# Optimization experiments

Hardware: AMD Instinct MI355X
Metric: run time of the kernel (lower is better)

Reference implementation:

```python
import jax, jax.numpy as jnp
import numpy as np

N = 100_000      # nodes
E = 1_600_000    # edges
F_IN = 64        # num_features
H = 64           # hidden_dim
G = 128          # graphs in batch
BN_EPS = 1e-5


def _gcn_conv(x, W, b, row, col, ew, n_nodes):
    """PyG GCNConv with edge weights, self-loops, symmetric normalization."""
    # add self loops (weight 1.0)
    loops = jnp.arange(n_nodes, dtype=row.dtype)
    r = jnp.concatenate([row, loops])
    c = jnp.concatenate([col, loops])
    w = jnp.concatenate([ew, jnp.ones((n_nodes,), ew.dtype)])
    # deg over destination (col), as in PyG gcn_norm
    deg = jax.ops.segment_sum(w, c, num_segments=n_nodes)
    dinv = jnp.where(deg > 0, jax.lax.rsqrt(deg), 0.0)
    norm = dinv[r] * w * dinv[c]          # [E+N]
    h = x @ W                             # [N, H] small GEMM
    msg = h[r] * norm[:, None]            # gather + scale, [E+N, H]
    out = jax.ops.segment_sum(msg, c, num_segments=n_nodes)  # scatter-add
    return out + b


def _bn_eval(x, gamma, beta, mean, var):
    return (x - mean) * jax.lax.rsqrt(var + BN_EPS) * gamma + beta


def setup_inputs() -> dict:
    key = jax.random.key(0)
    ks = jax.random.split(key, 10)
    x = jax.random.normal(ks[0], (N, F_IN), jnp.float32)
    edge_index = jax.random.randint(ks[1], (2, E), 0, N, dtype=jnp.int32)
    edge_weight = jax.random.uniform(ks[2], (E,), jnp.float32)
    batch = jnp.sort(jax.random.randint(ks[3], (N,), 0, G, dtype=jnp.int32))

    def lin(k, i, o):
        return jax.random.normal(k, (i, o), jnp.float32) / np.float32(np.sqrt(i))

    d = {
        "x": x, "edge_index": edge_index, "edge_weight": edge_weight, "batch": batch,
        "W1": lin(ks[4], F_IN, H), "b1": jnp.zeros((H,), jnp.float32),
        "W2": lin(ks[5], H, H),    "b2": jnp.zeros((H,), jnp.float32),
        "W3": lin(ks[6], H, H),    "b3": jnp.zeros((H,), jnp.float32),
        "Wfc": lin(ks[7], H, 1),   "bfc": jnp.zeros((1,), jnp.float32),
    }
    for i in (1, 2, 3):
        d[f"g{i}"] = jnp.ones((H,), jnp.float32)   # BN gamma
        d[f"be{i}"] = jnp.zeros((H,), jnp.float32)  # BN beta
        d[f"m{i}"] = jnp.zeros((H,), jnp.float32)   # BN running mean
        d[f"v{i}"] = jnp.ones((H,), jnp.float32)    # BN running var
    return d


def reference(x, edge_index, edge_weight, batch,
              W1, b1, W2, b2, W3, b3, Wfc, bfc,
              g1, be1, m1, v1, g2, be2, m2, v2, g3, be3, m3, v3):
    row, col = edge_index[0], edge_index[1]
    h = _gcn_conv(x, W1, b1, row, col, edge_weight, N)
    h = _bn_eval(jax.nn.relu(h), g1, be1, m1, v1)
    h = _gcn_conv(h, W2, b2, row, col, edge_weight, N)
    h = _bn_eval(jax.nn.relu(h), g2, be2, m2, v2)
    h = _gcn_conv(h, W3, b3, row, col, edge_weight, N)
    h = _bn_eval(h, g3, be3, m3, v3)               # note: no ReLU before bn3
    pooled = jax.ops.segment_sum(h, batch, num_segments=G)  # global_add_pool
    pooled = jax.nn.relu(pooled)                   # dropout is identity in eval
    return (pooled @ Wfc + bfc).reshape(-1)        # [G]
```

## Files before the change

### kernel.cpp

```cpp
#include <hip/hip_runtime.h>
#include <hip/hip_fp16.h>

#define BN_EPS 1e-5f
#define EPB 4096
#define PADCAP 4608
#define FP8_SCALE 16.0f
#define FP8_INV (1.0f / 16.0f)
#define W15_INV (1.0f / 32768.0f)
#define NPOOL 8

typedef __attribute__((ext_vector_type(2))) float vfloat2;
typedef __attribute__((ext_vector_type(8))) short short8;
typedef __attribute__((ext_vector_type(4))) float f32x4;

__device__ __forceinline__ float fatomic_add(float* p, float v) {
    return unsafeAtomicAdd(p, v);
}

__device__ __forceinline__ unsigned short f2bf(float f) {
    unsigned int u = __float_as_uint(f);
    return (unsigned short)((u + 0x7FFFu + ((u >> 16) & 1u)) >> 16);
}

__device__ __forceinline__ int xcd_swz(int bid, int nwg) {
    int xcd = bid & 7, k = bid >> 3;
    int q = nwg >> 3, r = nwg & 7;
    return (xcd < r ? xcd * (q + 1) : r * (q + 1) + (xcd - r) * q) + k;
}

__global__ __launch_bounds__(256) void k_wt(const float* __restrict__ W1,
                                            const float* __restrict__ W2,
                                            const float* __restrict__ W3,
                                            short* __restrict__ WT) {
    int tid = threadIdx.x;
    const float* Wm[3] = {W1, W2, W3};
#pragma unroll
    for (int m = 0; m < 3; ++m) {
        const float* W = Wm[m];
        short* o = WT + m * 4096;
        for (int i = tid; i < 4096; i += 256)
            o[i] = (short)f2bf(W[(i & 63) * 64 + (i >> 6)]);
    }
}

__global__ __launch_bounds__(256) void k_binscatter(const int* __restrict__ rowi,
                                                    const int* __restrict__ coli,
                                                    const float* __restrict__ ew,
                                                    unsigned int* __restrict__ binCursor,
                                                    int2* __restrict__ staged,
                                                    float* __restrict__ pooled8,
                                                    int E, int NB, int PZ) {
    __shared__ unsigned int h[512];
    __shared__ unsigned int bb[512];
    int tid = threadIdx.x;
    if (blockIdx.x == 0)
        for (int i = tid; i < PZ; i += 256) pooled8[i] = 0.f;
    for (int i = tid; i < 512; i += 256) h[i] = 0;
    __syncthreads();
    int base = blockIdx.x * EPB;
    int lim = min(EPB, E - base);
    unsigned short rank[16];
    int nj = (lim - tid + 255) / 256;
    for (int j = 0; j < nj; ++j) {
        int e = base + tid + j * 256;
        rank[j] = (unsigned short)atomicAdd(&h[(unsigned)coli[e] >> 8], 1u);
    }
    __syncthreads();
    for (int b = tid; b < NB; b += 256)
        bb[b] = h[b] ? atomicAdd(&binCursor[b], h[b]) : 0u;
    __syncthreads();
    for (int j = 0; j < nj; ++j) {
        int e = base + tid + j * 256;
        unsigned int c = (unsigned)coli[e];
        unsigned int b = c >> 8;
        int2 rec;
        rec.x = rowi[e] | (int)((c & 255u) << 24);
        rec.y = (int)min((unsigned int)(ew[e] * 32768.f + 0.5f), 32767u);
        staged[(size_t)b * PADCAP + bb[b] + rank[j]] = rec;
    }
}

__global__ __launch_bounds__(256) void k_binfinal(const int2* __restrict__ staged,
                                                  const unsigned int* __restrict__ binCursor,
                                                  unsigned int* __restrict__ csr,
                                                  int2* __restrict__ se,
                                                  float* __restrict__ dinv,
                                                  int N) {
    __shared__ int2 recs[PADCAP];
    __shared__ unsigned int cnt[256];
    __shared__ unsigned int deg[256];
    __shared__ int sc[256];
    __shared__ unsigned int cur[256];
    int tid = threadIdx.x;
    int b = blockIdx.x;
    int s0 = b * PADCAP;
    int n = (int)binCursor[b];
    cnt[tid] = 0;
    deg[tid] = 0;
    __syncthreads();
    for (int i = tid; i < n; i += 256) {
        int2 rec = staged[s0 + i];
        recs[i] = rec;
        unsigned int cl = (unsigned)rec.x >> 24;
        atomicAdd(&cnt[cl], 1u);
        atomicAdd(&deg[cl], (unsigned int)rec.y);
    }
    __syncthreads();
    int v = (int)cnt[tid];
    sc[tid] = v;
    __syncthreads();
    for (int off = 1; off < 256; off <<= 1) {
        int add = (tid >= off) ? sc[tid - off] : 0;
        __syncthreads();
        sc[tid] += add;
        __syncthreads();
    }
    int lpre = sc[tid] - v;
    cur[tid] = (unsigned int)lpre;
    int c = b * 256 + tid;
    if (c < N) {
        se[c] = make_int2(s0 + lpre, s0 + lpre + v);
        dinv[c] = rsqrtf(1.0f + (float)deg[tid] * W15_INV);
    }
    __syncthreads();
    for (int i = tid; i < n; i += 256) {
        int2 rec = recs[i];
        unsigned int cl = (unsigned)rec.x >> 24;
        unsigned int p = atomicAdd(&cur[cl], 1u);
        csr[s0 + p] = ((unsigned int)rec.y << 17) | ((unsigned)rec.x & 0x1FFFFu);
    }
}

__global__ __launch_bounds__(256) void k_gemm(const float* __restrict__ x,
                                              const short* __restrict__ WTg,
                                              const float* __restrict__ dinv,
                                              int* __restrict__ th4, int n) {
    __shared__ short Wt[64][72];
    __shared__ short xs[16][72];
    __shared__ float outs[16][68];
    int tid = threadIdx.x;
    {
        const int* WTi = (const int*)WTg;
        for (int i = tid; i < 2048; i += 256)
            *(int*)&Wt[i >> 5][(i & 31) * 2] = WTi[i];
    }
    int row0 = blockIdx.x * 16;
    int nrows = min(16, n - row0);
    {
        int r = tid >> 4, c4 = (tid & 15) * 4;
        float4 v = make_float4(0.f, 0.f, 0.f, 0.f);
        if (r < nrows)
            v = ((const float4*)(x + (size_t)(row0 + r) * 64))[tid & 15];
        xs[r][c4 + 0] = (short)f2bf(v.x);
        xs[r][c4 + 1] = (short)f2bf(v.y);
        xs[r][c4 + 2] = (short)f2bf(v.z);
        xs[r][c4 + 3] = (short)f2bf(v.w);
    }
    __syncthreads();
    int wv = tid >> 6, lane = tid & 63;
    int mn = lane & 15, kg = (lane >> 4) * 8;
    f32x4 acc = {0.f, 0.f, 0.f, 0.f};
    short8 a0 = *(const short8*)&xs[mn][kg];
    short8 a1 = *(const short8*)&xs[mn][kg + 32];
    short8 b0 = *(const short8*)&Wt[wv * 16 + mn][kg];
    short8 b1 = *(const short8*)&Wt[wv * 16 + mn][kg + 32];
    acc = __builtin_amdgcn_mfma_f32_16x16x32_bf16(a0, b0, acc, 0, 0, 0);
    acc = __builtin_amdgcn_mfma_f32_16x16x32_bf16(a1, b1, acc, 0, 0, 0);
#pragma unroll
    for (int r = 0; r < 4; ++r)
        outs[(lane >> 4) * 4 + r][wv * 16 + mn] = acc[r];
    __syncthreads();
    int rl = tid >> 4, fq = tid & 15;
    if (rl < nrows) {
        float d = dinv[row0 + rl] * FP8_SCALE;
        float4 o = *(const float4*)&outs[rl][fq * 4];
        int p = __builtin_amdgcn_cvt_pk_fp8_f32(o.x * d, o.y * d, 0, false);
        p = __builtin_amdgcn_cvt_pk_fp8_f32(o.z * d, o.w * d, p, true);
        th4[(row0 + rl) * 16 + fq] = p;
    }
}

__global__ __launch_bounds__(256) void k_fusedgg(const unsigned int* __restrict__ csr,
                                                 const int2* __restrict__ se,
                                                 const int* __restrict__ th4_in,
                                                 const float* __restrict__ dinv,
                                                 const float* __restrict__ bias,
                                                 const float* __restrict__ gam,
                                                 const float* __restrict__ bet,
                                                 const float* __restrict__ mu,
                                                 const float* __restrict__ var,
                                                 const short* __restrict__ WTg,
                                                 int* __restrict__ th4_out, int n) {
    __shared__ short Wt[64][72];
    __shared__ short xs[16][72];
    __shared__ float outs[16][68];
    int tid = threadIdx.x;
    {
        const int* WTi = (const int*)WTg;
        for (int i = tid; i < 2048; i += 256)
            *(int*)&Wt[i >> 5][(i & 31) * 2] = WTi[i];
    }
    int nb = xcd_swz(blockIdx.x, gridDim.x);
    int w = tid >> 6;
    int lane = tid & 63;
    int q = lane >> 4;
    int l = lane & 15;
    int node = nb * 16 + w * 4 + q;
    bool valid = node < n;
    float4 b4 = ((const float4*)bias)[l];
    float4 m4 = ((const float4*)mu)[l];
    float4 v4 = ((const float4*)var)[l];
    float4 G4 = ((const float4*)gam)[l];
    float4 B4 = ((const float4*)bet)[l];
    float4 scf, shf;
    scf.x = rsqrtf(v4.x + BN_EPS) * G4.x;  shf.x = B4.x - m4.x * scf.x;
    scf.y = rsqrtf(v4.y + BN_EPS) * G4.y;  shf.y = B4.y - m4.y * scf.y;
    scf.z = rsqrtf(v4.z + BN_EPS) * G4.z;  shf.z = B4.z - m4.z * scf.z;
    scf.w = rsqrtf(v4.w + BN_EPS) * G4.w;  shf.w = B4.w - m4.w * scf.w;

    float4 av[4];
    av[0] = make_float4(0.f, 0.f, 0.f, 0.f);
    av[1] = av[0]; av[2] = av[0]; av[3] = av[0];
    float4 sf = av[0];
    int e = 0, eend = 0;
    float dv = 0.f;
    if (valid) {
        int2 ext = se[node];
        e = ext.x; eend = ext.y;
        dv = dinv[node];
        int sv = th4_in[node * 16 + l];
        vfloat2 lo = __builtin_amdgcn_cvt_pk_f32_fp8(sv, false);
        vfloat2 hi = __builtin_amdgcn_cvt_pk_f32_fp8(sv, true);
        sf = make_float4(lo.x, lo.y, hi.x, hi.y);
    }
    while (__any(e < eend)) {
        if (e < eend) {
            unsigned int cc[8];
            int rr[8];
#pragma unroll
            for (int j = 0; j < 8; ++j)
                cc[j] = __builtin_nontemporal_load(&csr[e + j]);
#pragma unroll
            for (int j = 0; j < 8; ++j)
                rr[j] = th4_in[(int)((cc[j] & 0x1FFFFu) << 4) + l];
#pragma unroll
            for (int j = 0; j < 8; ++j) {
                float wj = (e + j < eend) ? (float)(cc[j] >> 17) : 0.f;
                vfloat2 lo = __builtin_amdgcn_cvt_pk_f32_fp8(rr[j], false);
                vfloat2 hi = __builtin_amdgcn_cvt_pk_f32_fp8(rr[j], true);
                av[j & 3].x = fmaf(wj, lo.x, av[j & 3].x);
                av[j & 3].y = fmaf(wj, lo.y, av[j & 3].y);
                av[j & 3].z = fmaf(wj, hi.x, av[j & 3].z);
                av[j & 3].w = fmaf(wj, hi.y, av[j & 3].w);
            }
        }
        e += 8;
    }
    float4 res = make_float4(0.f, 0.f, 0.f, 0.f);
    if (valid) {
        float4 acc;
        acc.x = ((av[0].x + av[1].x) + (av[2].x + av[3].x)) * W15_INV + sf.x;
        acc.y = ((av[0].y + av[1].y) + (av[2].y + av[3].y)) * W15_INV + sf.y;
        acc.z = ((av[0].z + av[1].z) + (av[2].z + av[3].z)) * W15_INV + sf.z;
        acc.w = ((av[0].w + av[1].w) + (av[2].w + av[3].w)) * W15_INV + sf.w;
        float d = dv * FP8_INV;
        float r0 = fmaxf(d * acc.x + b4.x, 0.f);
        float r1 = fmaxf(d * acc.y + b4.y, 0.f);
        float r2 = fmaxf(d * acc.z + b4.z, 0.f);
        float r3 = fmaxf(d * acc.w + b4.w, 0.f);
        res.x = r0 * scf.x + shf.x;
        res.y = r1 * scf.y + shf.y;
        res.z = r2 * scf.z + shf.z;
        res.w = r3 * scf.w + shf.w;
    }
    {
        int nl = w * 4 + q;
        union { unsigned short s[4]; int2 i2; } u;
        u.s[0] = f2bf(res.x); u.s[1] = f2bf(res.y);
        u.s[2] = f2bf(res.z); u.s[3] = f2bf(res.w);
        *(int2*)&xs[nl][4 * l] = u.i2;
    }
    __syncthreads();
    int mn = lane & 15, kg = (lane >> 4) * 8;
    f32x4 acc = {0.f, 0.f, 0.f, 0.f};
    short8 a0 = *(const short8*)&xs[mn][kg];
    short8 a1 = *(const short8*)&xs[mn][kg + 32];
    short8 b0 = *(const short8*)&Wt[w * 16 + mn][kg];
    short8 b1 = *(const short8*)&Wt[w * 16 + mn][kg + 32];
    acc = __builtin_amdgcn_mfma_f32_16x16x32_bf16(a0, b0, acc, 0, 0, 0);
    acc = __builtin_amdgcn_mfma_f32_16x16x32_bf16(a1, b1, acc, 0, 0, 0);
#pragma unroll
    for (int r = 0; r < 4; ++r)
        outs[(lane >> 4) * 4 + r][w * 16 + mn] = acc[r];
    __syncthreads();
    int rl = tid >> 4, fq = tid & 15;
    int row = nb * 16 + rl;
    if (row < n) {
        float d = dinv[row] * FP8_SCALE;
        float4 o = *(const float4*)&outs[rl][fq * 4];
        int p = __builtin_amdgcn_cvt_pk_fp8_f32(o.x * d, o.y * d, 0, false);
        p = __builtin_amdgcn_cvt_pk_fp8_f32(o.z * d, o.w * d, p, true);
        th4_out[row * 16 + fq] = p;
    }
}

__global__ __launch_bounds__(256) void k_gather(const unsigned int* __restrict__ csr,
                                                const int2* __restrict__ se,
                                                const int* __restrict__ th4,
                                                const float* __restrict__ dinv,
                                                const float* __restrict__ bias,
                                                const float* __restrict__ gam,
                                                const float* __restrict__ bet,
                                                const float* __restrict__ mu,
                                                const float* __restrict__ var,
                                                const int* __restrict__ batch,
                                                float* __restrict__ pooled8,
                                                int n, int G64) {
    __shared__ float vals[4][64];
    __shared__ int wbid[4];
    int nb = xcd_swz(blockIdx.x, gridDim.x);
    int w = threadIdx.x >> 6;
    int lane = threadIdx.x & 63;
    int q = lane >> 4;
    int l = lane & 15;
    int node = nb * 16 + w * 4 + q;
    bool valid = node < n;
    float* myPool = pooled8 + (size_t)(blockIdx.x & (NPOOL - 1)) * G64;
    float4 b4 = ((const float4*)bias)[l];
    float4 m4 = ((const float4*)mu)[l];
    float4 v4 = ((const float4*)var)[l];
    float4 G4 = ((const float4*)gam)[l];
    float4 B4 = ((const float4*)bet)[l];
    float4 scf, shf;
    scf.x = rsqrtf(v4.x + BN_EPS) * G4.x;  shf.x = B4.x - m4.x * scf.x;
    scf.y = rsqrtf(v4.y + BN_EPS) * G4.y;  shf.y = B4.y - m4.y * scf.y;
    scf.z = rsqrtf(v4.z + BN_EPS) * G4.z;  shf.z = B4.z - m4.z * scf.z;
    scf.w = rsqrtf(v4.w + BN_EPS) * G4.w;  shf.w = B4.w - m4.w * scf.w;

    float4 av[4];
    av[0] = make_float4(0.f, 0.f, 0.f, 0.f);
    av[1] = av[0]; av[2] = av[0]; av[3] = av[0];
    float4 sf = av[0];
    int e = 0, eend = 0;
    float dv = 0.f;
    if (valid) {
        int2 ext = se[node];
        e = ext.x; eend = ext.y;
        dv = dinv[node];
        int sv = th4[node * 16 + l];
        vfloat2 lo = __builtin_amdgcn_cvt_pk_f32_fp8(sv, false);
        vfloat2 hi = __builtin_amdgcn_cvt_pk_f32_fp8(sv, true);
        sf = make_float4(lo.x, lo.y, hi.x, hi.y);
    }
    while (__any(e < eend)) {
        if (e < eend) {
            unsigned int cc[8];
            int rr[8];
#pragma unroll
            for (int j = 0; j < 8; ++j)
                cc[j] = __builtin_nontemporal_load(&csr[e + j]);
#pragma unroll
            for (int j = 0; j < 8; ++j)
                rr[j] = th4[(int)((cc[j] & 0x1FFFFu) << 4) + l];
#pragma unroll
            for (int j = 0; j < 8; ++j) {
                float wj = (e + j < eend) ? (float)(cc[j] >> 17) : 0.f;
                vfloat2 lo = __builtin_amdgcn_cvt_pk_f32_fp8(rr[j], false);
                vfloat2 hi = __builtin_amdgcn_cvt_pk_f32_fp8(rr[j], true);
                av[j & 3].x = fmaf(wj, lo.x, av[j & 3].x);
                av[j & 3].y = fmaf(wj, lo.y, av[j & 3].y);
                av[j & 3].z = fmaf(wj, hi.x, av[j & 3].z);
                av[j & 3].w = fmaf(wj, hi.y, av[j & 3].w);
            }
        }
        e += 8;
    }
    float4 res = make_float4(0.f, 0.f, 0.f, 0.f);
    if (valid) {
        float4 acc;
        acc.x = ((av[0].x + av[1].x) + (av[2].x + av[3].x)) * W15_INV + sf.x;
        acc.y = ((av[0].y + av[1].y) + (av[2].y + av[3].y)) * W15_INV + sf.y;
        acc.z = ((av[0].z + av[1].z) + (av[2].z + av[3].z)) * W15_INV + sf.z;
        acc.w = ((av[0].w + av[1].w) + (av[2].w + av[3].w)) * W15_INV + sf.w;
        float d = dv * FP8_INV;
        float r0 = d * acc.x + b4.x;
        float r1 = d * acc.y + b4.y;
        float r2 = d * acc.z + b4.z;
        float r3 = d * acc.w + b4.w;
        res.x = r0 * scf.x + shf.x;
        res.y = r1 * scf.y + shf.y;
        res.z = r2 * scf.z + shf.z;
        res.w = r3 * scf.w + shf.w;
    }
    int bid = valid ? batch[node] : -1;
    int bid0 = __shfl(bid, 0);
    bool same = __all(bid == bid0);
    if (same) {
        res.x += __shfl_xor(res.x, 16);
        res.y += __shfl_xor(res.y, 16);
        res.z += __shfl_xor(res.z, 16);
        res.w += __shfl_xor(res.w, 16);
        res.x += __shfl_xor(res.x, 32);
        res.y += __shfl_xor(res.y, 32);
        res.z += __shfl_xor(res.z, 32);
        res.w += __shfl_xor(res.w, 32);
        if (q == 0) ((float4*)&vals[w][0])[l] = res;
        if (lane == 0) wbid[w] = bid0;
    } else {
        if (valid) {
            float* pp = myPool + bid * 64 + 4 * l;
            fatomic_add(pp + 0, res.x);
            fatomic_add(pp + 1, res.y);
            fatomic_add(pp + 2, res.z);
            fatomic_add(pp + 3, res.w);
        }
        if (lane == 0) wbid[w] = -1;
    }
    __syncthreads();
    if (w == 0) {
        int f = threadIdx.x;
        float s2 = 0.f;
        int cur = -1;
#pragma unroll
        for (int i = 0; i < 4; ++i) {
            int bi = wbid[i];
            if (bi < 0) continue;
            if (bi == cur) {
                s2 += vals[i][f];
            } else {
                if (cur >= 0) fatomic_add(&myPool[cur * 64 + f], s2);
                cur = bi;
                s2 = vals[i][f];
            }
        }
        if (cur >= 0) fatomic_add(&myPool[cur * 64 + f], s2);
    }
}

__global__ __launch_bounds__(64) void k_fc(const float* __restrict__ pooled8,
                                           const float* __restrict__ Wfc,
                                           const float* __restrict__ bfc,
                                           float* __restrict__ out, int G) {
    int g = blockIdx.x;
    int f = threadIdx.x;
    int G64 = G * 64;
    float p = 0.f;
#pragma unroll
    for (int c = 0; c < NPOOL; ++c) p += pooled8[c * G64 + g * 64 + f];
    float s = fmaxf(p, 0.f) * Wfc[f];
#pragma unroll
    for (int off = 1; off < 64; off <<= 1) s += __shfl_xor(s, off);
    if (f == 0) out[g] = s + bfc[0];
}

extern "C" void kernel_launch(void* const* d_in, const int* in_sizes, int n_in,
                              void* d_out, int out_size, void* d_ws, size_t ws_size,
                              hipStream_t stream) {
    const float* x    = (const float*)d_in[0];
    const int*   eidx = (const int*)d_in[1];
    const float* ew   = (const float*)d_in[2];
    const int*   batch= (const int*)d_in[3];
    const float* W1 = (const float*)d_in[4];
    const float* b1 = (const float*)d_in[5];
    const float* W2 = (const float*)d_in[6];
    const float* b2 = (const float*)d_in[7];
    const float* W3 = (const float*)d_in[8];
    const float* b3 = (const float*)d_in[9];
    const float* Wfc = (const float*)d_in[10];
    const float* bfc = (const float*)d_in[11];
    const float* g1 = (const float*)d_in[12];
    const float* be1 = (const float*)d_in[13];
    const float* m1 = (const float*)d_in[14];
    const float* v1 = (const float*)d_in[15];
    const float* g2 = (const float*)d_in[16];
    const float* be2 = (const float*)d_in[17];
    const float* m2 = (const float*)d_in[18];
    const float* v2 = (const float*)d_in[19];
    const float* g3 = (const float*)d_in[20];
    const float* be3 = (const float*)d_in[21];
    const float* m3 = (const float*)d_in[22];
    const float* v3 = (const float*)d_in[23];

    const int N = in_sizes[0] / 64;
    const int E = in_sizes[1] / 2;
    const int G = out_size;
    const int* rowi = eidx;
    const int* coli = eidx + E;
    const int NB = (N + 255) >> 8;

    char* ws = (char*)d_ws;
    size_t off = 0;
    auto alloc = [&](size_t bytes) {
        char* p = ws + off;
        off += (bytes + 255) & ~(size_t)255;
        return p;
    };
    unsigned int* binCursor = (unsigned int*)alloc(512 * 4);
    float* dinv   = (float*)alloc((size_t)N * 4);
    int2*  se     = (int2*) alloc((size_t)N * 8);
    unsigned int* csr = (unsigned int*)alloc((size_t)NB * PADCAP * 4 + 256);
    int*   th4a   = (int*)  alloc((size_t)N * 64);
    int*   th4b   = (int*)  alloc((size_t)N * 64);
    float* pooled8 = (float*)alloc((size_t)NPOOL * G * 64 * 4);
    short* wtg    = (short*)alloc(3 * 4096 * 2);
    int2*  staged = (int2*)alloc((size_t)NB * PADCAP * 8);

    const int bblk = (E + EPB - 1) / EPB;
    const int gblk = (N + 15) / 16;
    const int mblk = (N + 15) / 16;

    k_wt<<<1, 256, 0, stream>>>(W1, W2, W3, wtg);
    hipMemsetAsync(binCursor, 0, 512 * 4, stream);
    k_binscatter<<<bblk, 256, 0, stream>>>(rowi, coli, ew, binCursor, staged,
                                           pooled8, E, NB, NPOOL * G * 64);
    k_binfinal<<<NB, 256, 0, stream>>>(staged, binCursor, csr, se, dinv, N);

    k_gemm<<<mblk, 256, 0, stream>>>(x, wtg, dinv, th4a, N);
    k_fusedgg<<<gblk, 256, 0, stream>>>(csr, se, th4a, dinv, b1, g1, be1, m1, v1,
                                        wtg + 4096, th4b, N);
    k_fusedgg<<<gblk, 256, 0, stream>>>(csr, se, th4b, dinv, b2, g2, be2, m2, v2,
                                        wtg + 8192, th4a, N);
    k_gather<<<gblk, 256, 0, stream>>>(csr, se, th4a, dinv, b3, g3, be3, m3, v3,
                                       batch, pooled8, N, G * 64);
    k_fc<<<G, 64, 0, stream>>>(pooled8, Wfc, bfc, (float*)d_out, G);
}
```

Measured before the change: 310.4 us.

## Locally sort edges by bin in LDS before coalesced staged writes; fuse weight transpose

In the bin-scatter kernel, each block now runs a prefix scan over its per-bin counts and places its edges into a shared-memory buffer sorted by bin. It then writes them to the staged array in contiguous runs, replacing scattered 8-byte global stores with mostly coalesced ones. The bin id is packed into the weight field so the copy-out loop can find each record's destination, and the consumer masks those bits off. The separate weight-transpose kernel launch is folded into block 1 of this kernel, at the cost of extra LDS (about 32KB), which may lower occupancy.

```diff
diff --git a/kernel.cpp b/kernel.cpp
--- a/kernel.cpp
+++ b/kernel.cpp
@@ -28,33 +28,35 @@
     return (xcd < r ? xcd * (q + 1) : r * (q + 1) + (xcd - r) * q) + k;
 }
 
-__global__ __launch_bounds__(256) void k_wt(const float* __restrict__ W1,
-                                            const float* __restrict__ W2,
-                                            const float* __restrict__ W3,
-                                            short* __restrict__ WT) {
-    int tid = threadIdx.x;
-    const float* Wm[3] = {W1, W2, W3};
-#pragma unroll
-    for (int m = 0; m < 3; ++m) {
-        const float* W = Wm[m];
-        short* o = WT + m * 4096;
-        for (int i = tid; i < 4096; i += 256)
-            o[i] = (short)f2bf(W[(i & 63) * 64 + (i >> 6)]);
-    }
-}
-
 __global__ __launch_bounds__(256) void k_binscatter(const int* __restrict__ rowi,
                                                     const int* __restrict__ coli,
                                                     const float* __restrict__ ew,
                                                     unsigned int* __restrict__ binCursor,
                                                     int2* __restrict__ staged,
                                                     float* __restrict__ pooled8,
+                                                    const float* __restrict__ W1,
+                                                    const float* __restrict__ W2,
+                                                    const float* __restrict__ W3,
+                                                    short* __restrict__ WT,
                                                     int E, int NB, int PZ) {
     __shared__ unsigned int h[512];
-    __shared__ unsigned int bb[512];
+    __shared__ unsigned int lo[512];
+    __shared__ unsigned int dd[512];
+    __shared__ unsigned int ps[256];
+    __shared__ int2 lsorted[EPB];
     int tid = threadIdx.x;
-    if (blockIdx.x == 0)
+    if (blockIdx.x == 0) {
         for (int i = tid; i < PZ; i += 256) pooled8[i] = 0.f;
+    } else if (blockIdx.x == 1) {
+        const float* Wm[3] = {W1, W2, W3};
+#pragma unroll
+        for (int m = 0; m < 3; ++m) {
+            const float* W = Wm[m];
+            short* o = WT + m * 4096;
+            for (int i = tid; i < 4096; i += 256)
+                o[i] = (short)f2bf(W[(i & 63) * 64 + (i >> 6)]);
+        }
+    }
     for (int i = tid; i < 512; i += 256) h[i] = 0;
     __syncthreads();
     int base = blockIdx.x * EPB;
@@ -66,8 +68,23 @@
         rank[j] = (unsigned short)atomicAdd(&h[(unsigned)coli[e] >> 8], 1u);
     }
     __syncthreads();
-    for (int b = tid; b < NB; b += 256)
-        bb[b] = h[b] ? atomicAdd(&binCursor[b], h[b]) : 0u;
+    unsigned int a0 = h[2 * tid], a1 = h[2 * tid + 1];
+    ps[tid] = a0 + a1;
+    __syncthreads();
+    for (int off = 1; off < 256; off <<= 1) {
+        unsigned int add = (tid >= off) ? ps[tid - off] : 0u;
+        __syncthreads();
+        ps[tid] += add;
+        __syncthreads();
+    }
+    unsigned int excl = ps[tid] - (a0 + a1);
+    lo[2 * tid] = excl;
+    lo[2 * tid + 1] = excl + a0;
+    __syncthreads();
+    for (int b = tid; b < NB; b += 256) {
+        unsigned int bbv = h[b] ? atomicAdd(&binCursor[b], h[b]) : 0u;
+        dd[b] = (unsigned int)(b * PADCAP) + bbv - lo[b];
+    }
     __syncthreads();
     for (int j = 0; j < nj; ++j) {
         int e = base + tid + j * 256;
@@ -75,8 +92,15 @@
         unsigned int b = c >> 8;
         int2 rec;
         rec.x = rowi[e] | (int)((c & 255u) << 24);
-        rec.y = (int)min((unsigned int)(ew[e] * 32768.f + 0.5f), 32767u);
-        staged[(size_t)b * PADCAP + bb[b] + rank[j]] = rec;
+        unsigned int w15 = min((unsigned int)(ew[e] * 32768.f + 0.5f), 32767u);
+        rec.y = (int)(w15 | (b << 15));
+        lsorted[lo[b] + rank[j]] = rec;
+    }
+    __syncthreads();
+    for (int i = tid; i < lim; i += 256) {
+        int2 rec = lsorted[i];
+        unsigned int b = ((unsigned)rec.y >> 15) & 0x1FFu;
+        staged[dd[b] + i] = rec;
     }
 }
 
@@ -103,7 +127,7 @@
         recs[i] = rec;
         unsigned int cl = (unsigned)rec.x >> 24;
         atomicAdd(&cnt[cl], 1u);
-        atomicAdd(&deg[cl], (unsigned int)rec.y);
+        atomicAdd(&deg[cl], (unsigned int)rec.y & 0x7FFFu);
     }
     __syncthreads();
     int v = (int)cnt[tid];
@@ -127,7 +151,8 @@
         int2 rec = recs[i];
         unsigned int cl = (unsigned)rec.x >> 24;
         unsigned int p = atomicAdd(&cur[cl], 1u);
-        csr[s0 + p] = ((unsigned int)rec.y << 17) | ((unsigned)rec.x & 0x1FFFFu);
+        csr[s0 + p] = (((unsigned int)rec.y & 0x7FFFu) << 17) |
+                      ((unsigned)rec.x & 0x1FFFFu);
     }
 }
 
@@ -509,10 +534,10 @@
     const int gblk = (N + 15) / 16;
     const int mblk = (N + 15) / 16;
 
-    k_wt<<<1, 256, 0, stream>>>(W1, W2, W3, wtg);
     hipMemsetAsync(binCursor, 0, 512 * 4, stream);
     k_binscatter<<<bblk, 256, 0, stream>>>(rowi, coli, ew, binCursor, staged,
-                                           pooled8, E, NB, NPOOL * G * 64);
+                                           pooled8, W1, W2, W3, wtg,
+                                           E, NB, NPOOL * G * 64);
     k_binfinal<<<NB, 256, 0, stream>>>(staged, binCursor, csr, se, dinv, N);
 
     k_gemm<<<mblk, 256, 0, stream>>>(x, wtg, dinv, th4a, N);
```

Result: faster. 296.3 us (-4.6%).
